# Kernel tuning notes

Measured on AMD Instinct MI355X. Metric: run time of the kernel, lower is better.

## Reference

```python
import jax, jax.numpy as jnp
import numpy as np

N_NODES = 100000
N_EDGES = 1600000
IN_FEATS, HIDDEN, OUT_MU, OUT_LV = 256, 128, 64, 64


def setup_inputs() -> dict:
    key = jax.random.key(0)
    ks = jax.random.split(key, 8)
    X = jax.random.normal(ks[0], (N_NODES, IN_FEATS), dtype=jnp.float32)
    edge_index = jax.random.randint(ks[1], (2, N_EDGES), 0, N_NODES, dtype=jnp.int64)
    def glorot(k, shape):
        lim = np.sqrt(6.0 / (shape[0] + shape[1])).astype(np.float32)
        return jax.random.uniform(k, shape, jnp.float32, -lim, lim)
    W1 = glorot(ks[2], (IN_FEATS, HIDDEN))
    b1 = jnp.zeros((HIDDEN,), jnp.float32)
    Wmu = glorot(ks[3], (HIDDEN, OUT_MU))
    bmu = jnp.zeros((OUT_MU,), jnp.float32)
    Wlv = glorot(ks[4], (HIDDEN, OUT_LV))
    blv = jnp.zeros((OUT_LV,), jnp.float32)
    return {"X": X, "edge_index": edge_index, "W1": W1, "b1": b1,
            "Wmu": Wmu, "bmu": bmu, "Wlv": Wlv, "blv": blv}


def _gcn_norm(edge_index, num_nodes):
    # Add self-loops (PyG GCNConv default) and compute symmetric normalization.
    loop = jnp.arange(num_nodes, dtype=edge_index.dtype)
    row = jnp.concatenate([edge_index[0], loop])  # source
    col = jnp.concatenate([edge_index[1], loop])  # target
    deg = jax.ops.segment_sum(jnp.ones_like(col, dtype=jnp.float32), col,
                              num_segments=num_nodes)
    dinv = jnp.where(deg > 0, jax.lax.rsqrt(deg), 0.0)
    norm = dinv[row] * dinv[col]  # [E+N]
    return row, col, norm


def _gcn_conv(x, W, b, row, col, norm, num_nodes):
    # Linear transform, then normalized sparse neighbor aggregation at targets.
    h = x @ W                                   # [N, F_out]
    msg = h[row] * norm[:, None]                # gather + scale, [E+N, F_out]
    out = jax.ops.segment_sum(msg, col, num_segments=num_nodes)
    return out + b


def reference(X, edge_index, W1, b1, Wmu, bmu, Wlv, blv):
    n = X.shape[0]
    row, col, norm = _gcn_norm(edge_index, n)
    H = jax.nn.relu(_gcn_conv(X, W1, b1, row, col, norm, n))
    mu = _gcn_conv(H, Wmu, bmu, row, col, norm, n)
    lv = _gcn_conv(H, Wlv, blv, row, col, norm, n)
    return (mu, lv)
```

## Files before the change

kernel.cpp:

```cpp
#include <hip/hip_runtime.h>
#include <hip/hip_bf16.h>
#include <cstdint>

#define N_FEATS_IN 256
#define HID 128
#define OUTF 64
#define NBMAX 400
#define BCAP 6144
#define XS_STRIDE 264

typedef __bf16 bf16x8 __attribute__((ext_vector_type(8)));
typedef __bf16 bf16x4 __attribute__((ext_vector_type(4)));
typedef __bf16 bf16x2 __attribute__((ext_vector_type(2)));
typedef float f32x4 __attribute__((ext_vector_type(4)));


__global__ __launch_bounds__(256) void bucket_count(const int* __restrict__ ei, int E,
    int CH, int NB, int* __restrict__ gbk, int* __restrict__ bbase) {
  __shared__ int cnt[NBMAX];
  const int t = threadIdx.x, blk = blockIdx.x;
  for (int i = t; i < NB; i += 256) cnt[i] = 0;
  __syncthreads();
  int base = blk * CH, lim = min(base + CH, E);
  for (int i = base + t; i < lim; i += 256) atomicAdd(&cnt[ei[E + i] >> 8], 1);
  __syncthreads();
  for (int i = t; i < NB; i += 256) {
    int b = (i + blk) % NB;
    int v = cnt[b];
    bbase[(size_t)blk * NB + b] = (v > 0) ? atomicAdd(&gbk[b], v) : 0;
  }
}

__global__ __launch_bounds__(512) void bucket_scan(const int* __restrict__ gbk,
    int* __restrict__ gbkoff, int NB, int E) {
  __shared__ int ts[512];
  const int t = threadIdx.x;
  int v = (t < NB) ? gbk[t] : 0;
  ts[t] = v;
  __syncthreads();
  for (int off = 1; off < 512; off <<= 1) {
    int u = (t >= off) ? ts[t - off] : 0;
    __syncthreads();
    ts[t] += u;
    __syncthreads();
  }
  if (t < NB) gbkoff[t] = ts[t] - v;
  if (t == 0) gbkoff[NB] = E;
}

__global__ __launch_bounds__(256) void bucket_scatter(const int* __restrict__ ei, int E,
    int CH, int NB, const int* __restrict__ gbkoff, const int* __restrict__ bbase,
    int2* __restrict__ bucketed) {
  __shared__ int cur[NBMAX];
  const int t = threadIdx.x, blk = blockIdx.x;
  for (int i = t; i < NB; i += 256)
    cur[i] = gbkoff[i] + bbase[(size_t)blk * NB + i];
  __syncthreads();
  int base = blk * CH, lim = min(base + CH, E);
  for (int i = base + t; i < lim; i += 256) {
    int s = ei[i];
    int c = ei[E + i];
    int p = atomicAdd(&cur[c >> 8], 1);
    bucketed[p] = make_int2(s, c);
  }
}

__global__ __launch_bounds__(256) void bucket_csr(const int2* __restrict__ bucketed,
    const int* __restrict__ gbkoff, int NB, int N, int E,
    float* __restrict__ dinv, int* __restrict__ ptr, int* __restrict__ csrc) {
  __shared__ int2 eb[BCAP];
  __shared__ int cnt[256], scn[256], cur[256];
  const int b = blockIdx.x, t = threadIdx.x;
  const int beg = gbkoff[b], end = gbkoff[b + 1];
  const int M = end - beg;
  cnt[t] = 0;
  __syncthreads();
  const bool inlds = (M <= BCAP);
  if (inlds) {
    for (int i = t; i < M; i += 256) {
      int2 r = bucketed[beg + i];
      eb[i] = r;
      atomicAdd(&cnt[r.y & 255], 1);
    }
  } else {
    for (int i = t; i < M; i += 256) atomicAdd(&cnt[bucketed[beg + i].y & 255], 1);
  }
  __syncthreads();
  const int c0 = cnt[t];
  scn[t] = c0;
  __syncthreads();
  for (int off = 1; off < 256; off <<= 1) {
    int u = (t >= off) ? scn[t - off] : 0;
    __syncthreads();
    scn[t] += u;
    __syncthreads();
  }
  const int excl = scn[t] - c0;
  const int node = b * 256 + t;
  if (node < N) {
    ptr[node] = beg + excl;
    dinv[node] = rsqrtf((float)(c0 + 1));
  }
  if (b == NB - 1 && t == 0) ptr[N] = E;
  cur[t] = excl;
  __syncthreads();
  if (inlds) {
    for (int i = t; i < M; i += 256) {
      int2 r = eb[i];
      int slot = atomicAdd(&cur[r.y & 255], 1);
      csrc[beg + slot] = r.x;
    }
  } else {
    for (int i = t; i < M; i += 256) {
      int2 r = bucketed[beg + i];
      int slot = atomicAdd(&cur[r.y & 255], 1);
      csrc[beg + slot] = r.x;
    }
  }
}


__global__ __launch_bounds__(256) void pack_all_kernel(const float* __restrict__ W1,
    const float* __restrict__ Wmu, const float* __restrict__ Wlv,
    __bf16* __restrict__ W1p, __bf16* __restrict__ Wcp) {
  int idx = blockIdx.x * 256 + threadIdx.x;
  if (idx < 32768) {
    int j = idx & 7, l = (idx >> 3) & 63, t = (idx >> 9) & 7, s = idx >> 12;
    int k = s * 32 + (l >> 4) * 8 + j;
    int n = t * 16 + (l & 15);
    W1p[idx] = (__bf16)W1[k * HID + n];
  } else if (idx < 49152) {
    int i2 = idx - 32768;
    int j = i2 & 7, l = (i2 >> 3) & 63, t = (i2 >> 9) & 7, s = i2 >> 12;
    int k = s * 32 + (l >> 4) * 8 + j;
    int g = t * 16 + (l & 15);
    float v = (g < OUTF) ? Wmu[k * OUTF + g] : Wlv[k * OUTF + (g - OUTF)];
    Wcp[i2] = (__bf16)v;
  }
}


__global__ __launch_bounds__(256) void gemm1_mfma(const float* __restrict__ X,
    const __bf16* __restrict__ Wp, __bf16* __restrict__ Yb, int nrows) {
  __shared__ __bf16 xs[128 * XS_STRIDE];
  const int tid = threadIdx.x;
  const int rowbase = blockIdx.x * 128;

#pragma unroll
  for (int i = 0; i < 32; ++i) {
    int idx = i * 256 + tid;
    int row = idx >> 6;
    int cc = idx & 63;
    int gr = min(rowbase + row, nrows - 1);
    float4 v = ((const float4*)(X + (size_t)gr * N_FEATS_IN))[cc];
    bf16x4 b;
    b[0] = (__bf16)v.x; b[1] = (__bf16)v.y; b[2] = (__bf16)v.z; b[3] = (__bf16)v.w;
    *(bf16x4*)(xs + row * XS_STRIDE + cc * 4) = b;
  }
  __syncthreads();

  const int lane = tid & 63;
  const int wave = tid >> 6;
  const int lm = lane & 15;
  const int q = lane >> 4;
  const bf16x8* wp = (const bf16x8*)Wp;

  f32x4 acc[2][8];
#pragma unroll
  for (int m = 0; m < 2; ++m)
#pragma unroll
    for (int t = 0; t < 8; ++t) acc[m][t] = (f32x4)0.f;

#pragma unroll
  for (int s = 0; s < 8; ++s) {
    bf16x8 a0 = *(const bf16x8*)(xs + (wave * 32 + lm) * XS_STRIDE + s * 32 + q * 8);
    bf16x8 a1 = *(const bf16x8*)(xs + (wave * 32 + 16 + lm) * XS_STRIDE + s * 32 + q * 8);
#pragma unroll
    for (int t = 0; t < 8; ++t) {
      bf16x8 b = wp[(s * 8 + t) * 64 + lane];
      acc[0][t] = __builtin_amdgcn_mfma_f32_16x16x32_bf16(a0, b, acc[0][t], 0, 0, 0);
      acc[1][t] = __builtin_amdgcn_mfma_f32_16x16x32_bf16(a1, b, acc[1][t], 0, 0, 0);
    }
  }
#pragma unroll
  for (int m = 0; m < 2; ++m) {
    int rb = rowbase + wave * 32 + m * 16 + q * 4;
#pragma unroll
    for (int t = 0; t < 8; ++t) {
#pragma unroll
      for (int r2 = 0; r2 < 4; ++r2) {
        int row = rb + r2;
        if (row < nrows) Yb[(size_t)row * HID + t * 16 + lm] = (__bf16)acc[m][t][r2];
      }
    }
  }
}


__global__ __launch_bounds__(64) void agg_kernel(const __bf16* __restrict__ Fin,
    const int* __restrict__ ptr, const int* __restrict__ csrc,
    const float* __restrict__ dinv, const float* __restrict__ bias,
    __bf16* __restrict__ Fout, int do_relu) {
  const int c = blockIdx.x;
  const int t = threadIdx.x;
  const float d = dinv[c];
  bf16x2 sv = ((const bf16x2*)(Fin + (size_t)c * HID))[t];
  float ax = d * (float)sv[0];
  float ay = d * (float)sv[1];
  const int beg = ptr[c], end = ptr[c + 1];
  int e = beg;
  for (; e + 8 <= end; e += 8) {
    int r[8];
#pragma unroll
    for (int i = 0; i < 8; ++i) r[i] = csrc[e + i];
    float nr[8];
#pragma unroll
    for (int i = 0; i < 8; ++i) nr[i] = dinv[r[i]];
    bf16x2 v[8];
#pragma unroll
    for (int i = 0; i < 8; ++i) v[i] = ((const bf16x2*)(Fin + (size_t)r[i] * HID))[t];
#pragma unroll
    for (int i = 0; i < 8; ++i) {
      ax = fmaf(nr[i], (float)v[i][0], ax);
      ay = fmaf(nr[i], (float)v[i][1], ay);
    }
  }
  for (; e < end; ++e) {
    int r = csrc[e];
    float nr = dinv[r];
    bf16x2 v = ((const bf16x2*)(Fin + (size_t)r * HID))[t];
    ax = fmaf(nr, (float)v[0], ax);
    ay = fmaf(nr, (float)v[1], ay);
  }
  ax *= d;
  ay *= d;
  if (do_relu) {
    ax = fmaxf(ax + bias[2 * t], 0.f);
    ay = fmaxf(ay + bias[2 * t + 1], 0.f);
  }
  bf16x2 o;
  o[0] = (__bf16)ax;
  o[1] = (__bf16)ay;
  ((bf16x2*)(Fout + (size_t)c * HID))[t] = o;
}


__global__ __launch_bounds__(256) void gemm2_mfma(const __bf16* __restrict__ Gb,
    const __bf16* __restrict__ Wp, const float* __restrict__ bmu,
    const float* __restrict__ blv, float* __restrict__ out, int nrows, int ntiles) {
  __shared__ __bf16 bs[16384];
  const int tid = threadIdx.x;
  {
    const float4* s4 = (const float4*)Wp;
    float4* d4 = (float4*)bs;
#pragma unroll
    for (int i = 0; i < 8; ++i) d4[tid + 256 * i] = s4[tid + 256 * i];
  }
  __syncthreads();
  const int lane = tid & 63;
  const int wave = tid >> 6;
  const int lm = lane & 15;
  const int q = lane >> 4;
  const bf16x8* bsv = (const bf16x8*)bs;

  float bv[8];
  size_t obase[8];
#pragma unroll
  for (int t = 0; t < 8; ++t) {
    int col = t * 16 + lm;
    bv[t] = (col < OUTF) ? bmu[col] : blv[col - OUTF];
    obase[t] = (col < OUTF) ? (size_t)col : ((size_t)nrows * OUTF + (col - OUTF));
  }

  for (int tile = blockIdx.x; tile < ntiles; tile += gridDim.x) {
    const int row0 = tile * 64 + wave * 16;
    const int r = min(row0 + lm, nrows - 1);
    const bf16x8* gp = (const bf16x8*)(Gb + (size_t)r * HID);

    bf16x8 xa[4];
#pragma unroll
    for (int s = 0; s < 4; ++s) xa[s] = gp[s * 4 + q];

    f32x4 acc[8];
#pragma unroll
    for (int t = 0; t < 8; ++t) acc[t] = (f32x4)0.f;

#pragma unroll
    for (int s = 0; s < 4; ++s) {
#pragma unroll
      for (int t = 0; t < 8; ++t)
        acc[t] = __builtin_amdgcn_mfma_f32_16x16x32_bf16(xa[s], bsv[(s * 8 + t) * 64 + lane],
                                                         acc[t], 0, 0, 0);
    }
#pragma unroll
    for (int t = 0; t < 8; ++t) {
#pragma unroll
      for (int r2 = 0; r2 < 4; ++r2) {
        int row = row0 + q * 4 + r2;
        if (row < nrows) out[obase[t] + (size_t)row * OUTF] = acc[t][r2] + bv[t];
      }
    }
  }
}


extern "C" void kernel_launch(void* const* d_in, const int* in_sizes, int n_in,
                              void* d_out, int out_size, void* d_ws, size_t ws_size,
                              hipStream_t stream) {
  const float* X   = (const float*)d_in[0];
  const int*   ei  = (const int*)d_in[1];
  const float* W1  = (const float*)d_in[2];
  const float* b1  = (const float*)d_in[3];
  const float* Wmu = (const float*)d_in[4];
  const float* bmu = (const float*)d_in[5];
  const float* Wlv = (const float*)d_in[6];
  const float* blv = (const float*)d_in[7];
  float* out = (float*)d_out;

  const int N = in_sizes[0] / N_FEATS_IN;
  const int E = in_sizes[1] / 2;

  char* ws = (char*)d_ws;
  size_t off = 0;
  auto alloc = [&](size_t bytes) -> void* {
    void* p = ws + off;
    off += (bytes + 255) & ~(size_t)255;
    return p;
  };
  __bf16* Yb   = (__bf16*)alloc((size_t)N * HID * 2);
  __bf16* Hb   = (__bf16*)alloc((size_t)N * HID * 2);
  float* dinv  = (float*)alloc((size_t)N * 4);
  int*   ptr   = (int*)alloc((size_t)(N + 1) * 4);
  int2*  bucketed = (int2*)alloc((size_t)E * 8);
  int*   csrc  = (int*)alloc((size_t)E * 4);
  int*   gbk   = (int*)alloc((size_t)NBMAX * 4);
  int*   gbkoff = (int*)alloc((size_t)(NBMAX + 1) * 4);
  int*   bbase = (int*)alloc((size_t)256 * NBMAX * 4);
  __bf16* W1p  = (__bf16*)alloc(32768 * 2);
  __bf16* Wcp  = (__bf16*)alloc(16384 * 2);
  (void)ws_size; (void)n_in; (void)out_size;

  const int NB = (N + 255) >> 8;
  const int P = 256;
  const int CH = (E + P - 1) / P;

  hipMemsetAsync(gbk, 0, (size_t)NB * 4, stream);
  bucket_count<<<P, 256, 0, stream>>>(ei, E, CH, NB, gbk, bbase);
  bucket_scan<<<1, 512, 0, stream>>>(gbk, gbkoff, NB, E);
  bucket_scatter<<<P, 256, 0, stream>>>(ei, E, CH, NB, gbkoff, bbase, bucketed);
  bucket_csr<<<NB, 256, 0, stream>>>(bucketed, gbkoff, NB, N, E, dinv, ptr, csrc);
  pack_all_kernel<<<192, 256, 0, stream>>>(W1, Wmu, Wlv, W1p, Wcp);

  int g1 = (N + 127) / 128;
  gemm1_mfma<<<g1, 256, 0, stream>>>(X, W1p, Yb, N);
  agg_kernel<<<N, 64, 0, stream>>>(Yb, ptr, csrc, dinv, b1, Hb, 1);
  agg_kernel<<<N, 64, 0, stream>>>(Hb, ptr, csrc, dinv, b1, Yb, 0);
  int ntiles2 = (N + 63) / 64;
  int g2 = ntiles2 < 768 ? ntiles2 : 768;
  gemm2_mfma<<<g2, 256, 0, stream>>>(Yb, Wcp, bmu, blv, out, N, ntiles2);
}
```

Before: 404.8 us.

## Pre-scale rows by dinv and pack two nodes per wave in aggregation

The GEMM1 epilogue now multiplies each output row by dinv of its node. The aggregation kernels then sum pre-scaled neighbor rows directly, with no per-edge dinv gather. Layer-1 output is multiplied by dinv again after ReLU so layer 2 also reads pre-scaled rows. Aggregation also moves from one node per 64-thread block to two nodes per wave, with 4-element bf16 loads and 8 nodes per 256-thread block. This cuts per-edge random loads and launch granularity, but adds an extra bf16 rounding of scaled values.

```diff
diff --git a/kernel.cpp b/kernel.cpp
--- a/kernel.cpp
+++ b/kernel.cpp
@@ -141,7 +141,8 @@
 
 
 __global__ __launch_bounds__(256) void gemm1_mfma(const float* __restrict__ X,
-    const __bf16* __restrict__ Wp, __bf16* __restrict__ Yb, int nrows) {
+    const __bf16* __restrict__ Wp, const float* __restrict__ dinv,
+    __bf16* __restrict__ Yb, int nrows) {
   __shared__ __bf16 xs[128 * XS_STRIDE];
   const int tid = threadIdx.x;
   const int rowbase = blockIdx.x * 128;
@@ -182,6 +183,16 @@
       acc[1][t] = __builtin_amdgcn_mfma_f32_16x16x32_bf16(a1, b, acc[1][t], 0, 0, 0);
     }
   }
+
+  float dd[2][4];
+#pragma unroll
+  for (int m = 0; m < 2; ++m)
+#pragma unroll
+    for (int r2 = 0; r2 < 4; ++r2) {
+      int row = rowbase + wave * 32 + m * 16 + q * 4 + r2;
+      dd[m][r2] = (row < nrows) ? dinv[row] : 0.f;
+    }
+
 #pragma unroll
   for (int m = 0; m < 2; ++m) {
     int rb = rowbase + wave * 32 + m * 16 + q * 4;
@@ -190,58 +201,67 @@
 #pragma unroll
       for (int r2 = 0; r2 < 4; ++r2) {
         int row = rb + r2;
-        if (row < nrows) Yb[(size_t)row * HID + t * 16 + lm] = (__bf16)acc[m][t][r2];
+        if (row < nrows)
+          Yb[(size_t)row * HID + t * 16 + lm] = (__bf16)(acc[m][t][r2] * dd[m][r2]);
       }
     }
   }
 }
 
 
-__global__ __launch_bounds__(64) void agg_kernel(const __bf16* __restrict__ Fin,
+__global__ __launch_bounds__(256) void agg_kernel(const __bf16* __restrict__ Fin,
     const int* __restrict__ ptr, const int* __restrict__ csrc,
     const float* __restrict__ dinv, const float* __restrict__ bias,
-    __bf16* __restrict__ Fout, int do_relu) {
-  const int c = blockIdx.x;
-  const int t = threadIdx.x;
+    __bf16* __restrict__ Fout, int do_relu, int N) {
+  const int tid = threadIdx.x;
+  const int lane = tid & 63;
+  const int half = lane >> 5;
+  const int l = lane & 31;
+  const int c = blockIdx.x * 8 + (tid >> 6) * 2 + half;
+  if (c >= N) return;
+
   const float d = dinv[c];
-  bf16x2 sv = ((const bf16x2*)(Fin + (size_t)c * HID))[t];
-  float ax = d * (float)sv[0];
-  float ay = d * (float)sv[1];
+  bf16x4 sv = ((const bf16x4*)(Fin + (size_t)c * HID))[l];
+  float a0 = (float)sv[0], a1 = (float)sv[1], a2 = (float)sv[2], a3 = (float)sv[3];
+
   const int beg = ptr[c], end = ptr[c + 1];
   int e = beg;
   for (; e + 8 <= end; e += 8) {
     int r[8];
 #pragma unroll
     for (int i = 0; i < 8; ++i) r[i] = csrc[e + i];
-    float nr[8];
-#pragma unroll
-    for (int i = 0; i < 8; ++i) nr[i] = dinv[r[i]];
-    bf16x2 v[8];
-#pragma unroll
-    for (int i = 0; i < 8; ++i) v[i] = ((const bf16x2*)(Fin + (size_t)r[i] * HID))[t];
+    bf16x4 v[8];
+#pragma unroll
+    for (int i = 0; i < 8; ++i) v[i] = ((const bf16x4*)(Fin + (size_t)r[i] * HID))[l];
 #pragma unroll
     for (int i = 0; i < 8; ++i) {
-      ax = fmaf(nr[i], (float)v[i][0], ax);
-      ay = fmaf(nr[i], (float)v[i][1], ay);
+      a0 += (float)v[i][0];
+      a1 += (float)v[i][1];
+      a2 += (float)v[i][2];
+      a3 += (float)v[i][3];
     }
   }
   for (; e < end; ++e) {
     int r = csrc[e];
-    float nr = dinv[r];
-    bf16x2 v = ((const bf16x2*)(Fin + (size_t)r * HID))[t];
-    ax = fmaf(nr, (float)v[0], ax);
-    ay = fmaf(nr, (float)v[1], ay);
-  }
-  ax *= d;
-  ay *= d;
+    bf16x4 v = ((const bf16x4*)(Fin + (size_t)r * HID))[l];
+    a0 += (float)v[0];
+    a1 += (float)v[1];
+    a2 += (float)v[2];
+    a3 += (float)v[3];
+  }
+
   if (do_relu) {
-    ax = fmaxf(ax + bias[2 * t], 0.f);
-    ay = fmaxf(ay + bias[2 * t + 1], 0.f);
-  }
-  bf16x2 o;
-  o[0] = (__bf16)ax;
-  o[1] = (__bf16)ay;
-  ((bf16x2*)(Fout + (size_t)c * HID))[t] = o;
+    float4 bv = ((const float4*)bias)[l];
+    a0 = fmaxf(fmaf(d, a0, bv.x), 0.f) * d;
+    a1 = fmaxf(fmaf(d, a1, bv.y), 0.f) * d;
+    a2 = fmaxf(fmaf(d, a2, bv.z), 0.f) * d;
+    a3 = fmaxf(fmaf(d, a3, bv.w), 0.f) * d;
+  } else {
+    a0 *= d; a1 *= d; a2 *= d; a3 *= d;
+  }
+  bf16x4 o;
+  o[0] = (__bf16)a0; o[1] = (__bf16)a1; o[2] = (__bf16)a2; o[3] = (__bf16)a3;
+  ((bf16x4*)(Fout + (size_t)c * HID))[l] = o;
 }
 
 
@@ -352,9 +372,10 @@
   pack_all_kernel<<<192, 256, 0, stream>>>(W1, Wmu, Wlv, W1p, Wcp);
 
   int g1 = (N + 127) / 128;
-  gemm1_mfma<<<g1, 256, 0, stream>>>(X, W1p, Yb, N);
-  agg_kernel<<<N, 64, 0, stream>>>(Yb, ptr, csrc, dinv, b1, Hb, 1);
-  agg_kernel<<<N, 64, 0, stream>>>(Hb, ptr, csrc, dinv, b1, Yb, 0);
+  gemm1_mfma<<<g1, 256, 0, stream>>>(X, W1p, dinv, Yb, N);
+  int ga = (N + 7) / 8;
+  agg_kernel<<<ga, 256, 0, stream>>>(Yb, ptr, csrc, dinv, b1, Hb, 1, N);
+  agg_kernel<<<ga, 256, 0, stream>>>(Hb, ptr, csrc, dinv, b1, Yb, 0, N);
   int ntiles2 = (N + 63) / 64;
   int g2 = ntiles2 < 768 ? ntiles2 : 768;
   gemm2_mfma<<<g2, 256, 0, stream>>>(Yb, Wcp, bmu, blv, out, N, ntiles2);
```

Result: no change. 409.7 us (+1.2%).
